# Kernel optimization log

Hardware: AMD Instinct MI355X
Metric: run time of the kernel (lower is better)

Reference implementation:

```python
import jax, jax.numpy as jnp
import numpy as np

BLOCK = 32          # MXFP block size (OCP microscaling)
EMAX_FP4 = 2.0      # max exponent of FP4 E2M1 (max value 6.0 = 1.5 * 2^2)
FP4_MAX = 6.0       # saturation value of E2M1
E8M0_MIN, E8M0_MAX = -127.0, 127.0


def _quant_dequant_mxfp(t, block_dim):
    """Fake-quantize tensor t to MXFP4 (E2M1 elements, shared E8M0 scale per
    block of 32 along block_dim), then dequantize back to float."""
    t = jnp.moveaxis(t, block_dim, -1)
    shape = t.shape
    nb = shape[-1] // BLOCK
    tb = t.reshape(shape[:-1] + (nb, BLOCK))

    # shared power-of-two scale from block absmax: scale = 2^(floor(log2 amax) - emax)
    amax = jnp.max(jnp.abs(tb), axis=-1, keepdims=True)
    safe_amax = jnp.where(amax > 0, amax, 1.0)
    shared_exp = jnp.floor(jnp.log2(safe_amax)) - EMAX_FP4
    scale = jnp.exp2(jnp.clip(shared_exp, E8M0_MIN, E8M0_MAX))

    v = tb / scale
    sign = jnp.sign(v)
    a = jnp.clip(jnp.abs(v), 0.0, FP4_MAX)  # saturate to E2M1 max
    # E2M1 quantization step: 0.5 for |v|<2 (incl. subnormals), 1 for [2,4), 2 for [4,6]
    e = jnp.clip(jnp.floor(jnp.log2(jnp.maximum(a, 2.0 ** -10))), 0.0, EMAX_FP4)
    step = jnp.exp2(e - 1.0)
    q = jnp.round(a / step) * step

    deq = (sign * q * scale).reshape(shape)
    return jnp.moveaxis(deq, -1, block_dim)


def setup_inputs() -> dict:
    key = jax.random.key(0)
    kx, kw, kb = jax.random.split(key, 3)
    x = jax.random.normal(kx, (64, 4096), dtype=jnp.float32)
    weight = jax.random.normal(kw, (11008, 4096), dtype=jnp.float32) * 0.02
    bias = jax.random.normal(kb, (11008,), dtype=jnp.float32) * 0.02
    return {"x": x, "weight": weight, "bias": bias}


def reference(x, weight, bias):
    # layer_type = 'XqWqBq': MXFP4 quant-dequant on x (last dim), w (in_features
    # dim, block_dim=1) and b (dim 0), fused with the linear GEMM.
    x_dq = _quant_dequant_mxfp(x, block_dim=-1)        # [T, Din]
    w_dq = _quant_dequant_mxfp(weight, block_dim=1)    # [Dout, Din]
    b_dq = _quant_dequant_mxfp(bias, block_dim=0)      # [Dout]
    return jnp.einsum('ti,oi->to', x_dq, w_dq) + b_dq  # [T, Dout]
```

## Files before the change

kernel.cpp:

```cpp
#include <hip/hip_runtime.h>
#include <hip/hip_bf16.h>

#define DIN    4096
#define DOUT   11008
#define TM     64
#define KSPLIT 4
#define KCHUNK (DIN / KSPLIT)
#define NCHUNKS (DOUT / 16)

typedef __attribute__((ext_vector_type(8))) short  bf16x8;
typedef __attribute__((ext_vector_type(4))) float  f32x4;

__device__ inline void mx_consts(float amax, float& s2, float& s4, float& s6,
                                 float& m05, float& m1, float& m2) {
    float safe = amax > 0.0f ? amax : 1.0f;
    int e  = (int)((__float_as_uint(safe) >> 23) & 255) - 127;
    int se = e - 2;
    if (se < -127) se = -127;
    float scale = ldexpf(1.0f, se);
    s2  = scale + scale;
    s4  = s2 + s2;
    s6  = s4 + s2;
    m05 = ldexpf(scale, 22);
    m1  = m05 + m05;
    m2  = m1 + m1;
}

__device__ inline float mx_qd2(float v, float s2, float s4, float s6,
                               float m05, float m1, float m2) {
    float a  = fminf(fabsf(v), s6);
    float mg = (a < s2) ? m05 : ((a < s4) ? m1 : m2);
    float q  = (a + mg) - mg;
    return copysignf(q, v);
}

__device__ inline short bf16_trunc(float f) {
    return (short)(__float_as_uint(f) >> 16);
}

__device__ inline float blk_absmax8(const f32x4& a, const f32x4& b) {
    return fmaxf(fmaxf(fmaxf(fabsf(a[0]), fabsf(a[1])), fmaxf(fabsf(a[2]), fabsf(a[3]))),
                 fmaxf(fmaxf(fabsf(b[0]), fabsf(b[1])), fmaxf(fabsf(b[2]), fabsf(b[3]))));
}

__global__ __launch_bounds__(256) void quant_x_kernel(const float* __restrict__ x,
                                                      unsigned short* __restrict__ x_dq) {
    int gid = blockIdx.x * 256 + threadIdx.x;
    const float4 v = *(const float4*)(x + (size_t)gid * 4);
    float am = fmaxf(fmaxf(fabsf(v.x), fabsf(v.y)), fmaxf(fabsf(v.z), fabsf(v.w)));
    am = fmaxf(am, __shfl_xor(am, 1));
    am = fmaxf(am, __shfl_xor(am, 2));
    am = fmaxf(am, __shfl_xor(am, 4));
    float s2, s4, s6, m05, m1, m2;
    mx_consts(am, s2, s4, s6, m05, m1, m2);
    ushort4 q;
    q.x = (unsigned short)bf16_trunc(mx_qd2(v.x, s2, s4, s6, m05, m1, m2));
    q.y = (unsigned short)bf16_trunc(mx_qd2(v.y, s2, s4, s6, m05, m1, m2));
    q.z = (unsigned short)bf16_trunc(mx_qd2(v.z, s2, s4, s6, m05, m1, m2));
    q.w = (unsigned short)bf16_trunc(mx_qd2(v.w, s2, s4, s6, m05, m1, m2));
    *(ushort4*)(x_dq + (size_t)gid * 4) = q;
}

__global__ __launch_bounds__(256) void gemm_kernel(const unsigned short* __restrict__ x_dq,
                                                   const float* __restrict__ wgt,
                                                   float* __restrict__ partial) {
    const int lane  = threadIdx.x & 63;
    const int wid   = threadIdx.x >> 6;
    const int w     = blockIdx.x * 4 + wid;
    const int nch   = w % NCHUNKS;
    const int split = w / NCHUNKS;
    const int nlo   = lane & 15;
    const int kq    = lane >> 4;
    const int kbase = split * KCHUNK + kq * 8;

    const float*          wp = wgt  + (size_t)(nch * 16 + nlo) * DIN + kbase;
    const unsigned short* xp = x_dq + (size_t)nlo * DIN + kbase;

    f32x4 acc0 = {0.f,0.f,0.f,0.f};
    f32x4 acc1 = {0.f,0.f,0.f,0.f};
    f32x4 acc2 = {0.f,0.f,0.f,0.f};
    f32x4 acc3 = {0.f,0.f,0.f,0.f};

    f32x4 wa0 = *(const f32x4*)(wp);
    f32x4 wa1 = *(const f32x4*)(wp + 4);
    f32x4 wb0 = *(const f32x4*)(wp + 32);
    f32x4 wb1 = *(const f32x4*)(wp + 36);
    bf16x8 aa0 = *(const bf16x8*)(xp);
    bf16x8 aa1 = *(const bf16x8*)(xp + 16 * DIN);
    bf16x8 aa2 = *(const bf16x8*)(xp + 32 * DIN);
    bf16x8 aa3 = *(const bf16x8*)(xp + 48 * DIN);
    float s2, s4, s6, m05, m1, m2;
    {
        float am = blk_absmax8(wa0, wa1);
        am = fmaxf(am, __shfl_xor(am, 16));
        am = fmaxf(am, __shfl_xor(am, 32));
        mx_consts(am, s2, s4, s6, m05, m1, m2);
    }

    #pragma unroll 2
    for (int kk = 0; kk < KCHUNK; kk += 32) {
        const int kw = (kk + 64 < KCHUNK) ? kk + 64 : KCHUNK - 32;
        const int ka = (kk + 32 < KCHUNK) ? kk + 32 : KCHUNK - 32;
        f32x4 wc0 = *(const f32x4*)(wp + kw);
        f32x4 wc1 = *(const f32x4*)(wp + kw + 4);
        bf16x8 ab0 = *(const bf16x8*)(xp + ka);
        bf16x8 ab1 = *(const bf16x8*)(xp + 16 * DIN + ka);
        bf16x8 ab2 = *(const bf16x8*)(xp + 32 * DIN + ka);
        bf16x8 ab3 = *(const bf16x8*)(xp + 48 * DIN + ka);

        bf16x8 bf;
        bf[0] = bf16_trunc(mx_qd2(wa0[0], s2, s4, s6, m05, m1, m2));
        bf[1] = bf16_trunc(mx_qd2(wa0[1], s2, s4, s6, m05, m1, m2));
        bf[2] = bf16_trunc(mx_qd2(wa0[2], s2, s4, s6, m05, m1, m2));
        bf[3] = bf16_trunc(mx_qd2(wa0[3], s2, s4, s6, m05, m1, m2));
        bf[4] = bf16_trunc(mx_qd2(wa1[0], s2, s4, s6, m05, m1, m2));
        bf[5] = bf16_trunc(mx_qd2(wa1[1], s2, s4, s6, m05, m1, m2));
        bf[6] = bf16_trunc(mx_qd2(wa1[2], s2, s4, s6, m05, m1, m2));
        bf[7] = bf16_trunc(mx_qd2(wa1[3], s2, s4, s6, m05, m1, m2));

        acc0 = __builtin_amdgcn_mfma_f32_16x16x32_bf16(aa0, bf, acc0, 0, 0, 0);
        acc1 = __builtin_amdgcn_mfma_f32_16x16x32_bf16(aa1, bf, acc1, 0, 0, 0);
        acc2 = __builtin_amdgcn_mfma_f32_16x16x32_bf16(aa2, bf, acc2, 0, 0, 0);
        acc3 = __builtin_amdgcn_mfma_f32_16x16x32_bf16(aa3, bf, acc3, 0, 0, 0);

        float amn = blk_absmax8(wb0, wb1);
        amn = fmaxf(amn, __shfl_xor(amn, 16));
        amn = fmaxf(amn, __shfl_xor(amn, 32));
        mx_consts(amn, s2, s4, s6, m05, m1, m2);

        wa0 = wb0; wa1 = wb1;
        wb0 = wc0; wb1 = wc1;
        aa0 = ab0; aa1 = ab1; aa2 = ab2; aa3 = ab3;
    }

    float* pp = partial + (size_t)split * (TM * DOUT) + (size_t)(nch * 16 + nlo);
    const int mrow = kq * 4;
    #pragma unroll
    for (int r = 0; r < 4; ++r) {
        pp[(size_t)(mrow + r) * DOUT]      = acc0[r];
        pp[(size_t)(16 + mrow + r) * DOUT] = acc1[r];
        pp[(size_t)(32 + mrow + r) * DOUT] = acc2[r];
        pp[(size_t)(48 + mrow + r) * DOUT] = acc3[r];
    }
}

__global__ __launch_bounds__(256) void reduce_bias_kernel(const float* __restrict__ partial,
                                                          const float* __restrict__ bias,
                                                          float* __restrict__ out) {
    int gid = blockIdx.x * 256 + threadIdx.x;
    float s = 0.f;
    #pragma unroll
    for (int i = 0; i < KSPLIT; ++i)
        s += partial[(size_t)i * (TM * DOUT) + gid];
    int n = gid % DOUT;
    float v = bias[n];
    float am = fabsf(v);
    am = fmaxf(am, __shfl_xor(am, 1));
    am = fmaxf(am, __shfl_xor(am, 2));
    am = fmaxf(am, __shfl_xor(am, 4));
    am = fmaxf(am, __shfl_xor(am, 8));
    am = fmaxf(am, __shfl_xor(am, 16));
    float s2, s4, s6, m05, m1, m2;
    mx_consts(am, s2, s4, s6, m05, m1, m2);
    out[gid] = s + mx_qd2(v, s2, s4, s6, m05, m1, m2);
}

extern "C" void kernel_launch(void* const* d_in, const int* in_sizes, int n_in,
                              void* d_out, int out_size, void* d_ws, size_t ws_size,
                              hipStream_t stream) {
    const float* x    = (const float*)d_in[0];
    const float* wgt  = (const float*)d_in[1];
    const float* bias = (const float*)d_in[2];
    float* out = (float*)d_out;

    unsigned short* x_dq    = (unsigned short*)d_ws;
    float*          partial = (float*)((char*)d_ws + 512 * 1024);

    quant_x_kernel<<<256, 256, 0, stream>>>(x, x_dq);
    gemm_kernel<<<NCHUNKS * KSPLIT / 4, 256, 0, stream>>>(x_dq, wgt, partial);
    reduce_bias_kernel<<<TM * DOUT / 256, 256, 0, stream>>>(partial, bias, out);
}
```

Before: 289.0 us.

## Tile x_dq by K-block, double split-K, and stagger per-wave K start

The quantized activation buffer is now stored tiled by 32-wide K blocks, so each wave's four MFMA A-fragments come from one contiguous 4 KB tile instead of rows strided by DIN. Split-K is doubled to 8, which doubles the number of waves for more parallelism but also doubles the partial-sum traffic in the reduce kernel. Each wave starts its K loop at a rotated phase so that concurrent waves read different x tiles and weight columns, aiming to spread cache and channel pressure. The pipelined prefetch logic is kept but now wraps modulo the tiles per split.

```diff
diff --git a/kernel.cpp b/kernel.cpp
--- a/kernel.cpp
+++ b/kernel.cpp
@@ -4,8 +4,9 @@
 #define DIN    4096
 #define DOUT   11008
 #define TM     64
-#define KSPLIT 4
+#define KSPLIT 8
 #define KCHUNK (DIN / KSPLIT)
+#define TPS    (KCHUNK / 32)
 #define NCHUNKS (DOUT / 16)
 
 typedef __attribute__((ext_vector_type(8))) short  bf16x8;
@@ -44,7 +45,7 @@
 }
 
 __global__ __launch_bounds__(256) void quant_x_kernel(const float* __restrict__ x,
-                                                      unsigned short* __restrict__ x_dq) {
+                                                      unsigned short* __restrict__ x_t) {
     int gid = blockIdx.x * 256 + threadIdx.x;
     const float4 v = *(const float4*)(x + (size_t)gid * 4);
     float am = fmaxf(fmaxf(fabsf(v.x), fabsf(v.y)), fmaxf(fabsf(v.z), fabsf(v.w)));
@@ -58,10 +59,15 @@
     q.y = (unsigned short)bf16_trunc(mx_qd2(v.y, s2, s4, s6, m05, m1, m2));
     q.z = (unsigned short)bf16_trunc(mx_qd2(v.z, s2, s4, s6, m05, m1, m2));
     q.w = (unsigned short)bf16_trunc(mx_qd2(v.w, s2, s4, s6, m05, m1, m2));
-    *(ushort4*)(x_dq + (size_t)gid * 4) = q;
+    int c4 = gid * 4;
+    int r  = c4 >> 12;
+    int c  = c4 & 4095;
+    int kb = c >> 5;
+    int j  = c & 31;
+    *(ushort4*)(x_t + (size_t)kb * (64 * 32) + r * 32 + j) = q;
 }
 
-__global__ __launch_bounds__(256) void gemm_kernel(const unsigned short* __restrict__ x_dq,
+__global__ __launch_bounds__(256) void gemm_kernel(const unsigned short* __restrict__ x_t,
                                                    const float* __restrict__ wgt,
                                                    float* __restrict__ partial) {
     const int lane  = threadIdx.x & 63;
@@ -69,26 +75,30 @@
     const int w     = blockIdx.x * 4 + wid;
     const int nch   = w % NCHUNKS;
     const int split = w / NCHUNKS;
+    const int phase = (w * 11) & (TPS - 1);
     const int nlo   = lane & 15;
     const int kq    = lane >> 4;
-    const int kbase = split * KCHUNK + kq * 8;
 
-    const float*          wp = wgt  + (size_t)(nch * 16 + nlo) * DIN + kbase;
-    const unsigned short* xp = x_dq + (size_t)nlo * DIN + kbase;
+    const float*          wp = wgt + (size_t)(nch * 16 + nlo) * DIN + kq * 8;
+    const unsigned short* xt = x_t + nlo * 32 + kq * 8;
 
     f32x4 acc0 = {0.f,0.f,0.f,0.f};
     f32x4 acc1 = {0.f,0.f,0.f,0.f};
     f32x4 acc2 = {0.f,0.f,0.f,0.f};
     f32x4 acc3 = {0.f,0.f,0.f,0.f};
 
-    f32x4 wa0 = *(const f32x4*)(wp);
-    f32x4 wa1 = *(const f32x4*)(wp + 4);
-    f32x4 wb0 = *(const f32x4*)(wp + 32);
-    f32x4 wb1 = *(const f32x4*)(wp + 36);
-    bf16x8 aa0 = *(const bf16x8*)(xp);
-    bf16x8 aa1 = *(const bf16x8*)(xp + 16 * DIN);
-    bf16x8 aa2 = *(const bf16x8*)(xp + 32 * DIN);
-    bf16x8 aa3 = *(const bf16x8*)(xp + 48 * DIN);
+    auto kb_of = [&](int t) { return split * TPS + ((t + phase) & (TPS - 1)); };
+
+    const int kb0 = kb_of(0), kb1 = kb_of(1);
+    f32x4 wa0 = *(const f32x4*)(wp + kb0 * 32);
+    f32x4 wa1 = *(const f32x4*)(wp + kb0 * 32 + 4);
+    f32x4 wb0 = *(const f32x4*)(wp + kb1 * 32);
+    f32x4 wb1 = *(const f32x4*)(wp + kb1 * 32 + 4);
+    const unsigned short* xt0 = xt + (size_t)kb0 * 2048;
+    bf16x8 aa0 = *(const bf16x8*)(xt0);
+    bf16x8 aa1 = *(const bf16x8*)(xt0 + 512);
+    bf16x8 aa2 = *(const bf16x8*)(xt0 + 1024);
+    bf16x8 aa3 = *(const bf16x8*)(xt0 + 1536);
     float s2, s4, s6, m05, m1, m2;
     {
         float am = blk_absmax8(wa0, wa1);
@@ -97,16 +107,17 @@
         mx_consts(am, s2, s4, s6, m05, m1, m2);
     }
 
-    #pragma unroll 2
-    for (int kk = 0; kk < KCHUNK; kk += 32) {
-        const int kw = (kk + 64 < KCHUNK) ? kk + 64 : KCHUNK - 32;
-        const int ka = (kk + 32 < KCHUNK) ? kk + 32 : KCHUNK - 32;
-        f32x4 wc0 = *(const f32x4*)(wp + kw);
-        f32x4 wc1 = *(const f32x4*)(wp + kw + 4);
-        bf16x8 ab0 = *(const bf16x8*)(xp + ka);
-        bf16x8 ab1 = *(const bf16x8*)(xp + 16 * DIN + ka);
-        bf16x8 ab2 = *(const bf16x8*)(xp + 32 * DIN + ka);
-        bf16x8 ab3 = *(const bf16x8*)(xp + 48 * DIN + ka);
+    #pragma unroll 4
+    for (int t = 0; t < TPS; ++t) {
+        const int kbw = kb_of(t + 2 >= TPS ? t + 2 - TPS : t + 2);
+        const int kba = kb_of(t + 1 >= TPS ? t + 1 - TPS : t + 1);
+        f32x4 wc0 = *(const f32x4*)(wp + kbw * 32);
+        f32x4 wc1 = *(const f32x4*)(wp + kbw * 32 + 4);
+        const unsigned short* xta = xt + (size_t)kba * 2048;
+        bf16x8 ab0 = *(const bf16x8*)(xta);
+        bf16x8 ab1 = *(const bf16x8*)(xta + 512);
+        bf16x8 ab2 = *(const bf16x8*)(xta + 1024);
+        bf16x8 ab3 = *(const bf16x8*)(xta + 1536);
 
         bf16x8 bf;
         bf[0] = bf16_trunc(mx_qd2(wa0[0], s2, s4, s6, m05, m1, m2));
@@ -173,10 +184,10 @@
     const float* bias = (const float*)d_in[2];
     float* out = (float*)d_out;
 
-    unsigned short* x_dq    = (unsigned short*)d_ws;
+    unsigned short* x_t     = (unsigned short*)d_ws;
     float*          partial = (float*)((char*)d_ws + 512 * 1024);
 
-    quant_x_kernel<<<256, 256, 0, stream>>>(x, x_dq);
-    gemm_kernel<<<NCHUNKS * KSPLIT / 4, 256, 0, stream>>>(x_dq, wgt, partial);
+    quant_x_kernel<<<256, 256, 0, stream>>>(x, x_t);
+    gemm_kernel<<<NCHUNKS * KSPLIT / 4, 256, 0, stream>>>(x_t, wgt, partial);
     reduce_bias_kernel<<<TM * DOUT / 256, 256, 0, stream>>>(partial, bias, out);
 }
```

New measurement: 276.5 us. 4.3% less time.
